# Kernel optimization log

Hardware: AMD Instinct MI355X
Metric: run time of the kernel (lower is better)

## Reference

```python
import jax, jax.numpy as jnp
import numpy as np
import math

H = 16        # num_heads
HD = 64       # head_dim


def get_slopes(n):
    def pow2(n):
        start = 2 ** (-2 ** (-(math.log2(n) - 3)))
        return [start * start ** i for i in range(n)]
    if math.log2(n).is_integer():
        return pow2(n)
    c = 2 ** math.floor(math.log2(n))
    return pow2(c) + get_slopes(2 * c)[0::2][: n - c]


def setup_inputs() -> dict:
    key = jax.random.key(0)
    ks = jax.random.split(key, 6)
    b, n, d = 2, 2048, 1024
    s = 1.0 / math.sqrt(d)
    return {
        "x": jax.random.normal(ks[0], (b, n, d), jnp.float32),
        "Wq": jax.random.normal(ks[1], (d, d), jnp.float32) * s,
        "Wk": jax.random.normal(ks[2], (d, d), jnp.float32) * s,
        "Wv": jax.random.normal(ks[3], (d, d), jnp.float32) * s,
        "Wo": jax.random.normal(ks[4], (d, d), jnp.float32) * s,
        "bo": jnp.zeros((d,), jnp.float32),
    }


def reference(x, Wq, Wk, Wv, Wo, bo):
    b, n, d = x.shape
    # project and split heads: [b, H, n, HD]
    def heads(w):
        return (x @ w).reshape(b, n, H, HD).transpose(0, 2, 1, 3)
    q, k, v = heads(Wq), heads(Wk), heads(Wv)

    scores = jnp.einsum("bhqd,bhkd->bhqk", q, k)  # [b,H,n,n]
    pos = jnp.arange(n)
    dist = jnp.abs(pos[None, :] - pos[:, None]).astype(scores.dtype)  # [n,n]
    slopes = jnp.asarray(get_slopes(H), dtype=scores.dtype)
    scores = scores - slopes[:, None, None] * dist  # alibi subtracted BEFORE scaling (as in source)
    causal = pos[None, :] > pos[:, None]            # upper triangle masked
    scores = jnp.where(causal, -jnp.inf, scores)
    attn = jax.nn.softmax(scores / math.sqrt(HD), axis=-1)
    ctx = jnp.einsum("bhqk,bhkd->bhqd", attn, v)
    ctx = ctx.transpose(0, 2, 1, 3).reshape(b, n, d)
    return ctx @ Wo + bo
```

## Files before the change

### kernel.cpp

```cpp
#include <hip/hip_runtime.h>
#include <hip/hip_bf16.h>
#include <stdint.h>

#define NH 16
#define HDIM 64
#define NB 2
#define NSEQ 2048
#define DM 1024
#define MROWS (NB * NSEQ)

typedef __attribute__((ext_vector_type(8))) short bf16x8;
typedef __attribute__((ext_vector_type(4))) float f32x4;

#define MFMA32(a, b, c) __builtin_amdgcn_mfma_f32_16x16x32_bf16(a, b, c, 0, 0, 0)

static __device__ __forceinline__ unsigned short f2bf(float f) {
    union { float f; unsigned u; } v;
    v.f = f;
    unsigned r = v.u + 0x7fffu + ((v.u >> 16) & 1u);
    return (unsigned short)(r >> 16);
}

static __device__ __forceinline__ unsigned pack2bf(float a, float b) {
#if __has_builtin(__builtin_amdgcn_cvt_pk_bf16_f32)
    typedef __attribute__((ext_vector_type(2))) __bf16 bf2_t;
    union { bf2_t v; unsigned u; } c;
    c.v = __builtin_amdgcn_cvt_pk_bf16_f32(a, b);
    return c.u;
#else
    return (unsigned)f2bf(a) | ((unsigned)f2bf(b) << 16);
#endif
}

static __device__ __forceinline__ float fexp2(float x) {
#if __has_builtin(__builtin_amdgcn_exp2f)
    return __builtin_amdgcn_exp2f(x);
#else
    return exp2f(x);
#endif
}

typedef __attribute__((address_space(1))) void* gas_ptr;
typedef __attribute__((address_space(3))) void* las_ptr;

static __device__ __forceinline__ void load16_lds(const void* g, void* l) {
    __builtin_amdgcn_global_load_lds((gas_ptr)(uintptr_t)g, (las_ptr)(uintptr_t)l,
                                     16, 0, 0);
}

__global__ __launch_bounds__(256) void convert_kernel(
    const float* __restrict__ x,
    const float* __restrict__ wq, const float* __restrict__ wk,
    const float* __restrict__ wv, const float* __restrict__ wo,
    unsigned short* __restrict__ xb,
    unsigned short* __restrict__ wqkvt,
    unsigned short* __restrict__ wot)
{
    __shared__ unsigned short Ts[64][66];
    int t = threadIdx.x;
    int bx = blockIdx.x;
    if (bx < 1024) {
        const float4* xs = (const float4*)x + (long)bx * 1024;
        unsigned short* xd = xb + (long)bx * 4096;
#pragma unroll
        for (int i = 0; i < 4; i++) {
            float4 v = xs[i * 256 + t];
            ushort4 o;
            o.x = f2bf(v.x); o.y = f2bf(v.y); o.z = f2bf(v.z); o.w = f2bf(v.w);
            *(ushort4*)(xd + (i * 256 + t) * 4) = o;
        }
        return;
    }
    int wi = bx - 1024;
    int wsel = wi >> 8;
    int tile = wi & 255;
    int k0 = (tile >> 4) * 64, c0 = (tile & 15) * 64;
    const float* w = (wsel == 0) ? wq : (wsel == 1) ? wk : (wsel == 2) ? wv : wo;
    int lr = t >> 6, lc = t & 63;
#pragma unroll
    for (int rr = 0; rr < 16; rr++) {
        int row = rr * 4 + lr;
        Ts[row][lc] = f2bf(w[(long)(k0 + row) * DM + c0 + lc]);
    }
    __syncthreads();
    unsigned short* dst = (wsel == 3) ? wot : (wqkvt + (long)wsel * DM * DM);
#pragma unroll
    for (int rr = 0; rr < 16; rr++) {
        int crow = rr * 4 + lr;
        dst[(long)(c0 + crow) * DM + k0 + lc] = Ts[lc][crow];
    }
}

static __device__ __forceinline__ void gemm_tile_128(
    const unsigned short* __restrict__ A, const unsigned short* __restrict__ Bt,
    int m0, int n0, unsigned short* As, unsigned short* Bs, f32x4 (&acc)[4][4])
{
    int t = threadIdx.x;
    int lane = t & 63;
    int wave = t >> 6;
    int l16 = lane & 15, quad = lane >> 4;
    int wm = wave >> 1, wn = wave & 1;

    int off0 = t * 16;
    int off1 = off0 + 4096;
    const char* ga0 = (const char*)(A + (long)(m0 + (off0 >> 6)) * DM) + (off0 & 63);
    const char* ga1 = (const char*)(A + (long)(m0 + (off1 >> 6)) * DM) + (off1 & 63);
    const char* gb0 = (const char*)(Bt + (long)(n0 + (off0 >> 6)) * DM) + (off0 & 63);
    const char* gb1 = (const char*)(Bt + (long)(n0 + (off1 >> 6)) * DM) + (off1 & 63);
    char* sa0 = (char*)As + off0;
    char* sa1 = (char*)As + off1;
    char* sb0 = (char*)Bs + off0;
    char* sb1 = (char*)Bs + off1;

    const unsigned short* fa = As + (wm * 64 + l16) * 32 + quad * 8;
    const unsigned short* fb = Bs + (wn * 64 + l16) * 32 + quad * 8;

    for (int kk = 0; kk < DM; kk += 32) {
        load16_lds(ga0 + kk * 2, sa0);
        load16_lds(ga1 + kk * 2, sa1);
        load16_lds(gb0 + kk * 2, sb0);
        load16_lds(gb1 + kk * 2, sb1);
        __syncthreads();
        bf16x8 af[4], bf[4];
#pragma unroll
        for (int r = 0; r < 4; r++) af[r] = *(const bf16x8*)(fa + r * 16 * 32);
#pragma unroll
        for (int c = 0; c < 4; c++) bf[c] = *(const bf16x8*)(fb + c * 16 * 32);
#pragma unroll
        for (int r = 0; r < 4; r++)
#pragma unroll
            for (int c = 0; c < 4; c++)
                acc[r][c] = MFMA32(af[r], bf[c], acc[r][c]);
        __syncthreads();
    }
}

__global__ __launch_bounds__(256) void qkv_gemm_kernel(
    const unsigned short* __restrict__ A,
    const unsigned short* __restrict__ Bt,
    unsigned short* __restrict__ Qo, unsigned short* __restrict__ Ko,
    unsigned short* __restrict__ Vt)
{
    __shared__ unsigned short As[128 * 32];
    __shared__ unsigned short Bs[128 * 32];
    __shared__ unsigned short Tw[4][16][72];

    f32x4 acc[4][4] = {};
    int m0 = blockIdx.y * 128, n0 = blockIdx.x * 128;
    gemm_tile_128(A, Bt, m0, n0, As, Bs, acc);

    int t = threadIdx.x, wave = t >> 6, lane = t & 63;
    int l16 = lane & 15, quad = lane >> 4;
    int wm = wave >> 1, wn = wave & 1;
    int rg0 = m0 + wm * 64;
    int cg0 = n0 + wn * 64;
    int z = cg0 >> 10;
    int b_ = rg0 >> 11;
    int nb0 = rg0 & (NSEQ - 1);
    int h = (cg0 & 1023) >> 6;
    long bh = (long)(b_ * NH + h);

    if (z < 2) {
        unsigned short* dst = (z == 0 ? Qo : Ko) + bh * NSEQ * HDIM;
#pragma unroll
        for (int r = 0; r < 4; r++)
#pragma unroll
            for (int reg = 0; reg < 4; reg++) {
                long rowb = (long)(nb0 + r * 16 + quad * 4 + reg) * HDIM;
#pragma unroll
                for (int c = 0; c < 4; c++)
                    dst[rowb + c * 16 + l16] = f2bf(acc[r][c][reg]);
            }
    } else {
        unsigned short* dst = Vt + bh * HDIM * NSEQ;
#pragma unroll
        for (int c = 0; c < 4; c++) {
#pragma unroll
            for (int r = 0; r < 4; r++) {
                ushort4 u;
                u.x = f2bf(acc[r][c][0]); u.y = f2bf(acc[r][c][1]);
                u.z = f2bf(acc[r][c][2]); u.w = f2bf(acc[r][c][3]);
                *(ushort4*)&Tw[wave][l16][r * 16 + quad * 4] = u;
            }
#pragma unroll
            for (int j = 0; j < 4; j++) {
                int lrow = j * 4 + quad;
                ushort4 u = *(const ushort4*)&Tw[wave][lrow][l16 * 4];
                *(ushort4*)(dst + (long)(c * 16 + lrow) * NSEQ + nb0 + l16 * 4) = u;
            }
        }
    }
}

static __device__ __forceinline__ void stage_kv(
    const unsigned short* __restrict__ Kg,
    const unsigned short* __restrict__ Vtg,
    int kb, unsigned short* buf, int t)
{
#pragma unroll
    for (int r = 0; r < 2; r++) {
        int b = r * 256 + t;
        int row = b >> 3, sp = b & 7;
        int s = sp ^ (row & 7);
        load16_lds(Kg + (long)(kb + row) * HDIM + s * 8, buf + b * 8);
    }
#pragma unroll
    for (int r = 0; r < 2; r++) {
        int b = r * 256 + t;
        int row = b >> 3, sp = b & 7;
        int s = sp ^ (row & 7);
        load16_lds(Vtg + (long)row * NSEQ + kb + s * 8, buf + 4096 + b * 8);
    }
}

static __device__ __forceinline__ void softmax_fixed(
    f32x4* s, bool mask, int qb, int kb, float sc2, float mrow,
    f32x4& l_vec, unsigned pbu[2][4], int l16, int quad)
{
    if (mask) {
        int fdm = qb + l16 - kb - quad * 4;
#pragma unroll
        for (int tt = 0; tt < 4; tt++)
#pragma unroll
            for (int r = 0; r < 4; r++)
                if (tt * 16 + r > fdm) s[tt][r] = -3e38f;
    }
    f32x4 e[4];
#pragma unroll
    for (int tt = 0; tt < 4; tt++)
#pragma unroll
        for (int r = 0; r < 4; r++)
            e[tt][r] = fexp2(s[tt][r] * sc2 - mrow);
#pragma unroll
    for (int r = 0; r < 4; r++)
        l_vec[r] += (e[0][r] + e[1][r]) + (e[2][r] + e[3][r]);

#pragma unroll
    for (int p = 0; p < 2; p++) {
        pbu[p][0] = pack2bf(e[2 * p][0],     e[2 * p][1]);
        pbu[p][1] = pack2bf(e[2 * p][2],     e[2 * p][3]);
        pbu[p][2] = pack2bf(e[2 * p + 1][0], e[2 * p + 1][1]);
        pbu[p][3] = pack2bf(e[2 * p + 1][2], e[2 * p + 1][3]);
    }
}

__global__ __launch_bounds__(256) void attn_kernel(
    const unsigned short* __restrict__ Q,
    const unsigned short* __restrict__ K,
    const unsigned short* __restrict__ Vt,
    unsigned short* __restrict__ ctx)
{
    __shared__ unsigned short KV[2][8192];

    int t = threadIdx.x, w = t >> 6, lane = t & 63;
    int l16 = lane & 15, quad = lane >> 4;
    int r7 = l16 & 7;
    int bh = blockIdx.y;
    int b_ = bh >> 4, h = bh & 15;
    int pr = blockIdx.x;
    int t1 = 31 - pr, t0 = pr;
    int nch = t1 + 1;

    const unsigned short* Kg  = K  + (long)bh * NSEQ * HDIM;
    const unsigned short* Vtg = Vt + (long)bh * HDIM * NSEQ;

    const float log2e = 1.44269504f;
    float slope = exp2f(-0.5f * (float)(h + 1));
    float sc2 = 0.125f * log2e;
    float ss2 = slope * sc2;

    int qb1 = t1 * 64 + w * 16;
    int qb0 = t0 * 64 + w * 16;
    const unsigned short* qp1 = Q + ((long)bh * NSEQ + qb1 + l16) * HDIM + quad * 8;
    const unsigned short* qp0 = Q + ((long)bh * NSEQ + qb0 + l16) * HDIM + quad * 8;
    bf16x8 aq1_0 = *(const bf16x8*)qp1;
    bf16x8 aq1_1 = *(const bf16x8*)(qp1 + 32);
    bf16x8 aq0_0 = *(const bf16x8*)qp0;
    bf16x8 aq0_1 = *(const bf16x8*)(qp0 + 32);

    float mrow1 = ss2 * (float)(qb1 + l16);
    float mrow0 = ss2 * (float)(qb0 + l16);

    f32x4 cinit[4];
#pragma unroll
    for (int tt = 0; tt < 4; tt++)
#pragma unroll
        for (int r = 0; r < 4; r++)
            cinit[tt][r] = slope * (float)(tt * 16 + quad * 4 + r);
    float sl64 = slope * 64.0f;

    f32x4 l1v = {}, l0v = {};
    f32x4 o1[4] = {}, o0[4] = {};

    stage_kv(Kg, Vtg, 0, KV[0], t);

    for (int c = 0; c < nch; c++) {
        __syncthreads();
        if (c + 1 < nch) stage_kv(Kg, Vtg, (c + 1) * 64, KV[(c + 1) & 1], t);

        const unsigned short* Ks = KV[c & 1];
        const unsigned short* Vs = KV[c & 1] + 4096;
        int kb = c * 64;
        bool do0 = (c <= t0);

        f32x4 s1[4], s0[4];
#pragma unroll
        for (int tt = 0; tt < 4; tt++) {
            int rr = tt * 16 + l16;
            bf16x8 k0 = *(const bf16x8*)(Ks + (rr * 8 + (quad ^ r7)) * 8);
            bf16x8 k1 = *(const bf16x8*)(Ks + (rr * 8 + ((quad + 4) ^ r7)) * 8);
            f32x4 z1 = MFMA32(k0, aq1_0, cinit[tt]);
            s1[tt] = MFMA32(k1, aq1_1, z1);
            if (do0) {
                f32x4 z0 = MFMA32(k0, aq0_0, cinit[tt]);
                s0[tt] = MFMA32(k1, aq0_1, z0);
            }
        }

        unsigned pb1[2][4], pb0[2][4];
        softmax_fixed(s1, c == nch - 1, qb1, kb, sc2, mrow1, l1v, pb1, l16, quad);
        if (do0)
            softmax_fixed(s0, c == t0, qb0, kb, sc2, mrow0, l0v, pb0, l16, quad);

        int q2 = quad >> 1, q1b = (quad & 1) << 3;
#pragma unroll
        for (int cb = 0; cb < 4; cb++) {
            int rd = cb * 16 + l16;
            const char* vrow = (const char*)(Vs + rd * 64);
            int x7 = rd & 7;
#pragma unroll
            for (int p = 0; p < 2; p++) {
                union { bf16x8 v; uint2 u2[2]; } a;
                int sb0 = 4 * p + q2;
                int sb1 = 4 * p + 2 + q2;
                a.u2[0] = *(const uint2*)(vrow + ((sb0 ^ x7) << 4) + q1b);
                a.u2[1] = *(const uint2*)(vrow + ((sb1 ^ x7) << 4) + q1b);
                union { unsigned u[4]; bf16x8 v; } b1v;
#pragma unroll
                for (int i = 0; i < 4; i++) b1v.u[i] = pb1[p][i];
                o1[cb] = MFMA32(a.v, b1v.v, o1[cb]);
                if (do0) {
                    union { unsigned u[4]; bf16x8 v; } b0v;
#pragma unroll
                    for (int i = 0; i < 4; i++) b0v.u[i] = pb0[p][i];
                    o0[cb] = MFMA32(a.v, b0v.v, o0[cb]);
                }
            }
        }

#pragma unroll
        for (int tt = 0; tt < 4; tt++)
#pragma unroll
            for (int r = 0; r < 4; r++)
                cinit[tt][r] += sl64;
    }

    {
        float lt1 = (l1v[0] + l1v[1]) + (l1v[2] + l1v[3]);
        lt1 += __shfl_xor(lt1, 16);
        lt1 += __shfl_xor(lt1, 32);
        float lt0 = (l0v[0] + l0v[1]) + (l0v[2] + l0v[3]);
        lt0 += __shfl_xor(lt0, 16);
        lt0 += __shfl_xor(lt0, 32);
        float inv1 = 1.0f / lt1;
        float inv0 = 1.0f / lt0;
        long base1 = (((long)b_ * NSEQ + (qb1 + l16)) * NH + h) * HDIM + quad * 4;
        long base0 = (((long)b_ * NSEQ + (qb0 + l16)) * NH + h) * HDIM + quad * 4;
#pragma unroll
        for (int cb = 0; cb < 4; cb++) {
            uint2 u1, u0;
            u1.x = pack2bf(o1[cb][0] * inv1, o1[cb][1] * inv1);
            u1.y = pack2bf(o1[cb][2] * inv1, o1[cb][3] * inv1);
            u0.x = pack2bf(o0[cb][0] * inv0, o0[cb][1] * inv0);
            u0.y = pack2bf(o0[cb][2] * inv0, o0[cb][3] * inv0);
            *(uint2*)(ctx + base1 + cb * 16) = u1;
            *(uint2*)(ctx + base0 + cb * 16) = u0;
        }
    }
}

__global__ __launch_bounds__(256) void out_gemm_kernel(
    const unsigned short* __restrict__ A,
    const unsigned short* __restrict__ Bt,
    const float* __restrict__ bias,
    float* __restrict__ out)
{
    __shared__ unsigned short As[128 * 32];
    __shared__ unsigned short Bs[128 * 32];
    f32x4 acc[4][4] = {};
    int m0 = blockIdx.y * 128, n0 = blockIdx.x * 128;
    gemm_tile_128(A, Bt, m0, n0, As, Bs, acc);

    int t = threadIdx.x, wave = t >> 6, lane = t & 63;
    int l16 = lane & 15, quad = lane >> 4;
    int wm = wave >> 1, wn = wave & 1;
    int rg0 = m0 + wm * 64, cg0 = n0 + wn * 64;
#pragma unroll
    for (int c = 0; c < 4; c++) {
        float bc = bias[cg0 + c * 16 + l16];
#pragma unroll
        for (int r = 0; r < 4; r++)
#pragma unroll
            for (int reg = 0; reg < 4; reg++)
                out[(long)(rg0 + r * 16 + quad * 4 + reg) * DM + cg0 + c * 16 + l16] =
                    acc[r][c][reg] + bc;
    }
}

extern "C" void kernel_launch(void* const* d_in, const int* in_sizes, int n_in,
                              void* d_out, int out_size, void* d_ws, size_t ws_size,
                              hipStream_t stream)
{
    const float* x  = (const float*)d_in[0];
    const float* wq = (const float*)d_in[1];
    const float* wk = (const float*)d_in[2];
    const float* wv = (const float*)d_in[3];
    const float* wo = (const float*)d_in[4];
    const float* bo = (const float*)d_in[5];

    char* ws = (char*)d_ws;
    unsigned short* xb    = (unsigned short*)(ws);
    unsigned short* wqkvt = (unsigned short*)(ws + (8L  << 20));
    unsigned short* wot   = (unsigned short*)(ws + (14L << 20));
    unsigned short* Qb    = (unsigned short*)(ws + (16L << 20));
    unsigned short* Kb    = (unsigned short*)(ws + (24L << 20));
    unsigned short* Vt    = (unsigned short*)(ws + (32L << 20));
    unsigned short* ctx   = (unsigned short*)(ws + (40L << 20));
    float* out = (float*)d_out;

    convert_kernel<<<2048, 256, 0, stream>>>(x, wq, wk, wv, wo, xb, wqkvt, wot);

    qkv_gemm_kernel<<<dim3(3 * DM / 128, MROWS / 128), 256, 0, stream>>>(
        xb, wqkvt, Qb, Kb, Vt);

    attn_kernel<<<dim3(16, NB * NH), 256, 0, stream>>>(Qb, Kb, Vt, ctx);

    out_gemm_kernel<<<dim3(DM / 128, MROWS / 128), 256, 0, stream>>>(
        ctx, wot, bo, out);
}
```

Before: 202.8 us.

## Split attention into 32-row query tiles with per-wave tile ownership

The attention grid doubles to 32 blocks per head. Each block now pairs a 32-row query tile from the late half with one from the early half, and each wave owns a single 16-row tile instead of handling two. The ALiBi bias is applied by decrementing the row offset per chunk rather than updating the 16-register bias init. K/V staging addresses are precomputed, and block indices are swizzled across heads. The intent is more blocks in flight for better occupancy and balance, at the cost of reloading K/V in twice as many blocks and leaving the early-tile waves idle in late chunks.

```diff
diff --git a/kernel.cpp b/kernel.cpp
--- a/kernel.cpp
+++ b/kernel.cpp
@@ -192,27 +192,6 @@
     }
 }
 
-static __device__ __forceinline__ void stage_kv(
-    const unsigned short* __restrict__ Kg,
-    const unsigned short* __restrict__ Vtg,
-    int kb, unsigned short* buf, int t)
-{
-#pragma unroll
-    for (int r = 0; r < 2; r++) {
-        int b = r * 256 + t;
-        int row = b >> 3, sp = b & 7;
-        int s = sp ^ (row & 7);
-        load16_lds(Kg + (long)(kb + row) * HDIM + s * 8, buf + b * 8);
-    }
-#pragma unroll
-    for (int r = 0; r < 2; r++) {
-        int b = r * 256 + t;
-        int row = b >> 3, sp = b & 7;
-        int s = sp ^ (row & 7);
-        load16_lds(Vtg + (long)row * NSEQ + kb + s * 8, buf + 4096 + b * 8);
-    }
-}
-
 static __device__ __forceinline__ void softmax_fixed(
     f32x4* s, bool mask, int qb, int kb, float sc2, float mrow,
     f32x4& l_vec, unsigned pbu[2][4], int l16, int quad)
@@ -257,9 +236,12 @@
     int r7 = l16 & 7;
     int bh = blockIdx.y;
     int b_ = bh >> 4, h = bh & 15;
-    int pr = blockIdx.x;
-    int t1 = 31 - pr, t0 = pr;
-    int nch = t1 + 1;
+    int pr = (blockIdx.x + blockIdx.y) & 31;
+    int t1 = 63 - pr, t0 = pr;
+    int nch1 = (t1 >> 1) + 1;
+    int nch0 = (t0 >> 1) + 1;
+    int myNch = (w < 2) ? nch1 : nch0;
+    int qb = ((w < 2) ? t1 : t0) * 32 + (w & 1) * 16;
 
     const unsigned short* Kg  = K  + (long)bh * NSEQ * HDIM;
     const unsigned short* Vtg = Vt + (long)bh * HDIM * NSEQ;
@@ -268,18 +250,13 @@
     float slope = exp2f(-0.5f * (float)(h + 1));
     float sc2 = 0.125f * log2e;
     float ss2 = slope * sc2;
-
-    int qb1 = t1 * 64 + w * 16;
-    int qb0 = t0 * 64 + w * 16;
-    const unsigned short* qp1 = Q + ((long)bh * NSEQ + qb1 + l16) * HDIM + quad * 8;
-    const unsigned short* qp0 = Q + ((long)bh * NSEQ + qb0 + l16) * HDIM + quad * 8;
-    bf16x8 aq1_0 = *(const bf16x8*)qp1;
-    bf16x8 aq1_1 = *(const bf16x8*)(qp1 + 32);
-    bf16x8 aq0_0 = *(const bf16x8*)qp0;
-    bf16x8 aq0_1 = *(const bf16x8*)(qp0 + 32);
-
-    float mrow1 = ss2 * (float)(qb1 + l16);
-    float mrow0 = ss2 * (float)(qb0 + l16);
+    float ss2_64 = ss2 * 64.0f;
+
+    const unsigned short* qp = Q + ((long)bh * NSEQ + qb + l16) * HDIM + quad * 8;
+    bf16x8 aq0 = *(const bf16x8*)qp;
+    bf16x8 aq1 = *(const bf16x8*)(qp + 32);
+
+    float mr = ss2 * (float)(qb + l16);
 
     f32x4 cinit[4];
 #pragma unroll
@@ -287,40 +264,55 @@
 #pragma unroll
         for (int r = 0; r < 4; r++)
             cinit[tt][r] = slope * (float)(tt * 16 + quad * 4 + r);
-    float sl64 = slope * 64.0f;
-
-    f32x4 l1v = {}, l0v = {};
-    f32x4 o1[4] = {}, o0[4] = {};
-
-    stage_kv(Kg, Vtg, 0, KV[0], t);
-
-    for (int c = 0; c < nch; c++) {
+
+    f32x4 lv = {};
+    f32x4 o[4] = {};
+
+    int b0i = t, b1i = 256 + t;
+    int row0 = b0i >> 3, sw0 = (b0i & 7) ^ (row0 & 7);
+    int row1 = b1i >> 3, sw1 = (b1i & 7) ^ (row1 & 7);
+    const unsigned short* gk0 = Kg + row0 * HDIM + sw0 * 8;
+    const unsigned short* gk1 = Kg + row1 * HDIM + sw1 * 8;
+    const unsigned short* gv0 = Vtg + (long)row0 * NSEQ + sw0 * 8;
+    const unsigned short* gv1 = Vtg + (long)row1 * NSEQ + sw1 * 8;
+
+    {
+        unsigned short* buf = KV[0];
+        load16_lds(gk0, buf + b0i * 8);
+        load16_lds(gk1, buf + b1i * 8);
+        load16_lds(gv0, buf + 4096 + b0i * 8);
+        load16_lds(gv1, buf + 4096 + b1i * 8);
+    }
+
+    for (int c = 0; c < nch1; c++) {
         __syncthreads();
-        if (c + 1 < nch) stage_kv(Kg, Vtg, (c + 1) * 64, KV[(c + 1) & 1], t);
+        if (c + 1 < nch1) {
+            int kb2 = (c + 1) * 64;
+            unsigned short* buf = KV[(c + 1) & 1];
+            load16_lds(gk0 + kb2 * HDIM, buf + b0i * 8);
+            load16_lds(gk1 + kb2 * HDIM, buf + b1i * 8);
+            load16_lds(gv0 + kb2, buf + 4096 + b0i * 8);
+            load16_lds(gv1 + kb2, buf + 4096 + b1i * 8);
+        }
+        if (w >= 2 && c >= nch0) continue;
 
         const unsigned short* Ks = KV[c & 1];
         const unsigned short* Vs = KV[c & 1] + 4096;
         int kb = c * 64;
-        bool do0 = (c <= t0);
-
-        f32x4 s1[4], s0[4];
+
+        f32x4 s[4];
 #pragma unroll
         for (int tt = 0; tt < 4; tt++) {
             int rr = tt * 16 + l16;
             bf16x8 k0 = *(const bf16x8*)(Ks + (rr * 8 + (quad ^ r7)) * 8);
             bf16x8 k1 = *(const bf16x8*)(Ks + (rr * 8 + ((quad + 4) ^ r7)) * 8);
-            f32x4 z1 = MFMA32(k0, aq1_0, cinit[tt]);
-            s1[tt] = MFMA32(k1, aq1_1, z1);
-            if (do0) {
-                f32x4 z0 = MFMA32(k0, aq0_0, cinit[tt]);
-                s0[tt] = MFMA32(k1, aq0_1, z0);
-            }
-        }
-
-        unsigned pb1[2][4], pb0[2][4];
-        softmax_fixed(s1, c == nch - 1, qb1, kb, sc2, mrow1, l1v, pb1, l16, quad);
-        if (do0)
-            softmax_fixed(s0, c == t0, qb0, kb, sc2, mrow0, l0v, pb0, l16, quad);
+            f32x4 z = MFMA32(k0, aq0, cinit[tt]);
+            s[tt] = MFMA32(k1, aq1, z);
+        }
+
+        unsigned pb[2][4];
+        softmax_fixed(s, c == myNch - 1, qb, kb, sc2, mr, lv, pb, l16, quad);
+        mr -= ss2_64;
 
         int q2 = quad >> 1, q1b = (quad & 1) << 3;
 #pragma unroll
@@ -335,46 +327,26 @@
                 int sb1 = 4 * p + 2 + q2;
                 a.u2[0] = *(const uint2*)(vrow + ((sb0 ^ x7) << 4) + q1b);
                 a.u2[1] = *(const uint2*)(vrow + ((sb1 ^ x7) << 4) + q1b);
-                union { unsigned u[4]; bf16x8 v; } b1v;
-#pragma unroll
-                for (int i = 0; i < 4; i++) b1v.u[i] = pb1[p][i];
-                o1[cb] = MFMA32(a.v, b1v.v, o1[cb]);
-                if (do0) {
-                    union { unsigned u[4]; bf16x8 v; } b0v;
-#pragma unroll
-                    for (int i = 0; i < 4; i++) b0v.u[i] = pb0[p][i];
-                    o0[cb] = MFMA32(a.v, b0v.v, o0[cb]);
-                }
+                union { unsigned u[4]; bf16x8 v; } bv;
+#pragma unroll
+                for (int i = 0; i < 4; i++) bv.u[i] = pb[p][i];
+                o[cb] = MFMA32(a.v, bv.v, o[cb]);
             }
         }
-
-#pragma unroll
-        for (int tt = 0; tt < 4; tt++)
-#pragma unroll
-            for (int r = 0; r < 4; r++)
-                cinit[tt][r] += sl64;
     }
 
     {
-        float lt1 = (l1v[0] + l1v[1]) + (l1v[2] + l1v[3]);
-        lt1 += __shfl_xor(lt1, 16);
-        lt1 += __shfl_xor(lt1, 32);
-        float lt0 = (l0v[0] + l0v[1]) + (l0v[2] + l0v[3]);
-        lt0 += __shfl_xor(lt0, 16);
-        lt0 += __shfl_xor(lt0, 32);
-        float inv1 = 1.0f / lt1;
-        float inv0 = 1.0f / lt0;
-        long base1 = (((long)b_ * NSEQ + (qb1 + l16)) * NH + h) * HDIM + quad * 4;
-        long base0 = (((long)b_ * NSEQ + (qb0 + l16)) * NH + h) * HDIM + quad * 4;
+        float lt = (lv[0] + lv[1]) + (lv[2] + lv[3]);
+        lt += __shfl_xor(lt, 16);
+        lt += __shfl_xor(lt, 32);
+        float inv = 1.0f / lt;
+        long base = (((long)b_ * NSEQ + (qb + l16)) * NH + h) * HDIM + quad * 4;
 #pragma unroll
         for (int cb = 0; cb < 4; cb++) {
-            uint2 u1, u0;
-            u1.x = pack2bf(o1[cb][0] * inv1, o1[cb][1] * inv1);
-            u1.y = pack2bf(o1[cb][2] * inv1, o1[cb][3] * inv1);
-            u0.x = pack2bf(o0[cb][0] * inv0, o0[cb][1] * inv0);
-            u0.y = pack2bf(o0[cb][2] * inv0, o0[cb][3] * inv0);
-            *(uint2*)(ctx + base1 + cb * 16) = u1;
-            *(uint2*)(ctx + base0 + cb * 16) = u0;
+            uint2 u;
+            u.x = pack2bf(o[cb][0] * inv, o[cb][1] * inv);
+            u.y = pack2bf(o[cb][2] * inv, o[cb][3] * inv);
+            *(uint2*)(ctx + base + cb * 16) = u;
         }
     }
 }
@@ -433,7 +405,7 @@
     qkv_gemm_kernel<<<dim3(3 * DM / 128, MROWS / 128), 256, 0, stream>>>(
         xb, wqkvt, Qb, Kb, Vt);
 
-    attn_kernel<<<dim3(16, NB * NH), 256, 0, stream>>>(Qb, Kb, Vt, ctx);
+    attn_kernel<<<dim3(32, NB * NH), 256, 0, stream>>>(Qb, Kb, Vt, ctx);
 
     out_gemm_kernel<<<dim3(DM / 128, MROWS / 128), 256, 0, stream>>>(
         ctx, wot, bo, out);
```

Result: slower. 215.4 us (+6.2%).
